# Optimization experiments

Measured on AMD Instinct MI355X. Metric: run time of the kernel, lower is better.

Reference implementation:

```python
import jax, jax.numpy as jnp
import numpy as np

KERNEL_SIZE = 7       # NMS max-pool window
H, W = 512, 1024      # dims
TOP_K = 200
CIRCLE_RADIUS = 5
NUM_CLASSES = 34      # things are labelIds 24..33


def _circle_constants(radius):
    k = 2 * radius + 1
    ii, jj = np.meshgrid(np.arange(k), np.arange(k), indexing='ij')
    ox = (jj - radius).astype(np.float32)  # x offset of neighbor
    oy = (ii - radius).astype(np.float32)  # y offset of neighbor
    cd = np.sqrt(ox ** 2 + oy ** 2)
    cmask = (cd <= radius).astype(np.float32)
    n_pix = float(cmask.sum())
    thr = float((cd * cmask).sum() / n_pix)  # center_threshold buffer
    return ox, oy, cmask, n_pix, thr


def _vote_map(center_regressions, radius):
    # For each pixel p, average over circle neighbors q = p + o of ||o - reg(q)||
    # (get_patches with zero padding), then vote = -avg - 1.
    ox, oy, cmask, n_pix, thr = _circle_constants(radius)
    B, _, h, w = center_regressions.shape
    reg_p = jnp.pad(center_regressions, ((0, 0), (0, 0), (radius, radius), (radius, radius)))
    acc = jnp.zeros((B, h, w), center_regressions.dtype)
    k = 2 * radius + 1
    for i in range(k):          # fixed 11x11 window, ~97 in-circle taps
        for j in range(k):
            if cmask[i, j] == 0.0:
                continue
            rx = reg_p[:, 0, i:i + h, j:j + w]
            ry = reg_p[:, 1, i:i + h, j:j + w]
            acc = acc + jnp.sqrt((ox[i, j] - rx) ** 2 + (oy[i, j] - ry) ** 2)
    vote = -(acc / n_pix) - 1.0  # [B,H,W], always <= -1
    return vote, thr


def _forward(segmentation_logits, center_regressions):
    B = segmentation_logits.shape[0]
    seg_probs = jax.nn.softmax(segmentation_logits, axis=1)                # [B,C,H,W]
    seg_map = jnp.argmax(segmentation_logits, axis=1).astype(jnp.float32)  # [B,H,W]
    # Threshold(23.99, 50) then <= 33  <=>  23.99 < class <= 33
    things = (seg_map > 23.99) & (seg_map <= 33.0)
    # predicted absolute center per pixel; xy_coords are 1-based
    xg = jnp.arange(1, W + 1, dtype=jnp.float32)[None, None, :]
    yg = jnp.arange(1, H + 1, dtype=jnp.float32)[None, :, None]
    px = xg - center_regressions[:, 0]                                     # [B,H,W]
    py = yg - center_regressions[:, 1]
    vote, thr = _vote_map(center_regressions, CIRCLE_RADIUS)
    pooled = jax.lax.reduce_window(vote, -jnp.inf, jax.lax.max,
                                   (1, KERNEL_SIZE, KERNEL_SIZE), (1, 1, 1), 'SAME')
    keep = (pooled == vote) & (vote > -thr - 1.0)
    center_map = jnp.where(keep, vote, 0.0)                                # nms-ed vote map
    # top-k centers: surviving NMS positions ranked by aggregate vote value
    scores = jnp.where(center_map != 0.0, vote, -jnp.inf).reshape(B, -1)
    top_vals, top_idx = jax.lax.top_k(scores, TOP_K)                       # [B,K]
    ys = top_idx // W
    xs = top_idx % W
    valid = jnp.isfinite(top_vals)
    BIG = 1e9
    cx = jnp.where(valid, xs.astype(jnp.float32), BIG)
    cy = jnp.where(valid, ys.astype(jnp.float32), BIG)
    # nearest-center assignment; squared distance (argmin invariant under sqrt)
    d2 = (px[..., None] - cx[:, None, None, :]) ** 2 + (py[..., None] - cy[:, None, None, :]) ** 2
    inst_map = (jnp.argmin(d2, axis=-1).astype(jnp.int32) + 1) * things.astype(jnp.int32)
    return seg_probs, seg_map, center_map, inst_map, ys, xs, top_vals


def _instance_stats(inst_map, seg_map, seg_probs):
    # separate_inst_maps: per instance -> majority seg class, mean prob of that
    # class over the instance mask, and pixel count (vectorized via segment_sum)
    B = inst_map.shape[0]
    seg_ids = seg_map.astype(jnp.int32).reshape(B, -1)                     # [B,HW]
    inst_flat = inst_map.reshape(B, -1)                                    # [B,HW], 0 = background
    onehot = jax.nn.one_hot(seg_ids, NUM_CLASSES, dtype=jnp.float32)       # [B,HW,C]
    probs = jnp.transpose(seg_probs, (0, 2, 3, 1)).reshape(B, -1, NUM_CLASSES)
    seg_counts = jax.vmap(lambda v, s: jax.ops.segment_sum(v, s, num_segments=TOP_K + 1))(onehot, inst_flat)
    prob_sums = jax.vmap(lambda v, s: jax.ops.segment_sum(v, s, num_segments=TOP_K + 1))(probs, inst_flat)
    seg_counts = seg_counts[:, 1:]                                         # drop background -> [B,K,C]
    prob_sums = prob_sums[:, 1:]
    inst_size = seg_counts.sum(-1)                                         # [B,K]
    inst_class = jnp.argmax(seg_counts, axis=-1).astype(jnp.int32)         # [B,K]
    sel = jnp.take_along_axis(prob_sums, inst_class[..., None], axis=-1)[..., 0]
    inst_seg_prob = sel / jnp.maximum(inst_size, 1.0)
    return inst_class, inst_seg_prob, inst_size.astype(jnp.int32)


def setup_inputs() -> dict:
    key = jax.random.key(0)
    k1, k2, k3 = jax.random.split(key, 3)
    return {
        'segmentation_logits': jax.random.normal(k1, (2, NUM_CLASSES, H, W), jnp.float32),
        'center_maps_placeholder': jax.random.normal(k2, (2, 1, H, W), jnp.float32),
        'center_regressions': jax.random.normal(k3, (2, 2, H, W), jnp.float32),
    }


def reference(segmentation_logits, center_maps_placeholder, center_regressions):
    seg_probs, seg_map, center_map, inst_map, ys, xs, top_vals = _forward(
        segmentation_logits, center_regressions)
    inst_class, inst_seg_prob, inst_size = _instance_stats(inst_map, seg_map, seg_probs)
    centers = jnp.stack([ys, xs], -1).astype(jnp.int32)  # (row, col) like torch.nonzero
    return (inst_map, seg_map, centers, top_vals, inst_class, inst_seg_prob, inst_size, center_map)
```

## Files before the change

### kernel.cpp

```cpp
#include <hip/hip_runtime.h>
#include <cfloat>
#include <cmath>

#define NB 2
#define NC 34
#define NH 512
#define NW 1024
#define HWSZ (NH*NW)
#define TK 200
#define CAPC 49152
#define ACH 1024
#define NTH 10
#define ZWORDS (8 + NB*TK*NTH)

#define PST 1040
#define RPROWS 522
#define RPLEFT 8
#define VPROWS 518
#define VPLEFT 4
#define RPSZ (RPROWS*PST)
#define VPSZ (VPROWS*PST)

typedef unsigned long long u64;

#define PREP_ROWB (NB*2*RPROWS)
#define PREP_VF4 ((NB*VPSZ)/4)
#define PREP_VB ((PREP_VF4 + 255)/256)
#define PREP_ZB ((ZWORDS + NB*TK + 255)/256 + 1)
__global__ __launch_bounds__(256) void k_prep(const float* __restrict__ reg,
                                              float* __restrict__ reg_pad,
                                              float* __restrict__ vote_pad,
                                              int* __restrict__ zreg,
                                              float* __restrict__ o_iprob) {
    int bid = blockIdx.x;
    int tid = threadIdx.x;
    if (bid < PREP_ROWB) {
        int bc = bid / RPROWS;
        int r = bid % RPROWS;
        float* dst = reg_pad + (size_t)bc * RPSZ + (size_t)r * PST;
        if (r >= 5 && r < 517) {
            const float* src = reg + (size_t)bc * HWSZ + (size_t)(r - 5) * NW;
            *(float4*)(dst + RPLEFT + 4 * tid) = *(const float4*)(src + 4 * tid);
            if (tid < 2) *(float4*)(dst + 4 * tid) = make_float4(0.f, 0.f, 0.f, 0.f);
            else if (tid < 4) *(float4*)(dst + 1032 + 4 * (tid - 2)) = make_float4(0.f, 0.f, 0.f, 0.f);
        } else {
            for (int i = tid; i < PST / 4; i += 256)
                *(float4*)(dst + 4 * i) = make_float4(0.f, 0.f, 0.f, 0.f);
        }
    } else if (bid < PREP_ROWB + PREP_VB) {
        int idx4 = (bid - PREP_ROWB) * 256 + tid;
        if (idx4 < PREP_VF4)
            *(float4*)(vote_pad + (size_t)idx4 * 4) = make_float4(-INFINITY, -INFINITY, -INFINITY, -INFINITY);
    } else {
        int z = (bid - (PREP_ROWB + PREP_VB)) * 256 + tid;
        if (z < ZWORDS) zreg[z] = 0;
        else if (z < ZWORDS + NB * TK) o_iprob[z - ZWORDS] = 0.f;
    }
}

#define GETC(f, idx) (((idx)&3)==0 ? f[(idx)>>2].x : ((idx)&3)==1 ? f[(idx)>>2].y : \
                      ((idx)&3)==2 ? f[(idx)>>2].z : f[(idx)>>2].w)

__global__ __launch_bounds__(256, 4) void k_vote_seg(const float* __restrict__ reg_pad,
                                                     float* __restrict__ vote_pad,
                                                     const float* __restrict__ logits,
                                                     float* __restrict__ segmap_out,
                                                     float* __restrict__ mArr,
                                                     float* __restrict__ dArr) {
    int tid = threadIdx.x;
    int blk = blockIdx.x;
    int b = blk >> 9;
    int q = blk & 511;
    int y = ((q & 7) << 6) | (q >> 3);
    int xb = tid << 2;
    const float* rp0 = reg_pad + (size_t)(b * 2 + 0) * RPSZ;
    const float* rp1 = reg_pad + (size_t)(b * 2 + 1) * RPSZ;
    float a0 = 0.f, a1 = 0.f, a2 = 0.f, a3 = 0.f;

    float4 fA0[5], fA1[5], fB0[5], fB1[5];

    auto loadwin = [&](int i, float4* f0, float4* f1) {
        const float* p0 = rp0 + (size_t)(y + i) * PST + xb;
        const float* p1 = rp1 + (size_t)(y + i) * PST + xb;
#pragma unroll
        for (int t = 0; t < 5; t++) f0[t] = *(const float4*)(p0 + 4 * t);
#pragma unroll
        for (int t = 0; t < 5; t++) f1[t] = *(const float4*)(p1 + 4 * t);
    };

    auto compute = [&](int i, const float4* f0, const float4* f1) {
        int d = i - 5;
        int ad = d < 0 ? -d : d;
        int w = (int)sqrtf((float)(25 - ad * ad));
        int lo = 5 - w, hi = 5 + w;
        float di = (float)d;
#pragma unroll
        for (int j = 0; j < 11; j++) {
            if (j < lo || j > hi) continue;
            float dj = (float)(j - 5);
            float dx, dy, ss;
            dx = __fsub_rn(dj, GETC(f0, j+3)); dy = __fsub_rn(di, GETC(f1, j+3));
            ss = __fadd_rn(__fmul_rn(dx,dx), __fmul_rn(dy,dy));
            a0 = __fadd_rn(a0, sqrtf(ss));
            dx = __fsub_rn(dj, GETC(f0, j+4)); dy = __fsub_rn(di, GETC(f1, j+4));
            ss = __fadd_rn(__fmul_rn(dx,dx), __fmul_rn(dy,dy));
            a1 = __fadd_rn(a1, sqrtf(ss));
            dx = __fsub_rn(dj, GETC(f0, j+5)); dy = __fsub_rn(di, GETC(f1, j+5));
            ss = __fadd_rn(__fmul_rn(dx,dx), __fmul_rn(dy,dy));
            a2 = __fadd_rn(a2, sqrtf(ss));
            dx = __fsub_rn(dj, GETC(f0, j+6)); dy = __fsub_rn(di, GETC(f1, j+6));
            ss = __fadd_rn(__fmul_rn(dx,dx), __fmul_rn(dy,dy));
            a3 = __fadd_rn(a3, sqrtf(ss));
        }
    };

    loadwin(0, fA0, fA1);
#pragma unroll 1
    for (int i = 0; i < 10; i += 2) {
        loadwin(i + 1, fB0, fB1);
        compute(i, fA0, fA1);
        loadwin(i + 2, fA0, fA1);
        compute(i + 1, fB0, fB1);
    }
    compute(10, fA0, fA1);

    float4 vv;
    vv.x = __fsub_rn(-__fdiv_rn(a0, 81.0f), 1.0f);
    vv.y = __fsub_rn(-__fdiv_rn(a1, 81.0f), 1.0f);
    vv.z = __fsub_rn(-__fdiv_rn(a2, 81.0f), 1.0f);
    vv.w = __fsub_rn(-__fdiv_rn(a3, 81.0f), 1.0f);
    *(float4*)(vote_pad + (size_t)b * VPSZ + (size_t)(y + 3) * PST + (xb + VPLEFT)) = vv;

    const float* lg = logits + (size_t)b * NC * HWSZ + (size_t)y * NW + xb;
    float4 m4 = make_float4(-FLT_MAX, -FLT_MAX, -FLT_MAX, -FLT_MAX);
    float4 bc4 = make_float4(0.f, 0.f, 0.f, 0.f);
#pragma unroll
    for (int c = 0; c < NC; c++) {
        float4 v = *(const float4*)(lg + (size_t)c * HWSZ);
        if (v.x > m4.x) { m4.x = v.x; bc4.x = (float)c; }
        if (v.y > m4.y) { m4.y = v.y; bc4.y = (float)c; }
        if (v.z > m4.z) { m4.z = v.z; bc4.z = (float)c; }
        if (v.w > m4.w) { m4.w = v.w; bc4.w = (float)c; }
    }
    float4 den = make_float4(0.f, 0.f, 0.f, 0.f);
#pragma unroll
    for (int c = 0; c < NC; c++) {
        float4 v = *(const float4*)(lg + (size_t)c * HWSZ);
        den.x += expf(v.x - m4.x);
        den.y += expf(v.y - m4.y);
        den.z += expf(v.z - m4.z);
        den.w += expf(v.w - m4.w);
    }
    size_t po = (size_t)b * HWSZ + (size_t)y * NW + xb;
    *(float4*)(segmap_out + po) = bc4;
    *(float4*)(mArr + po) = m4;
    *(float4*)(dArr + po) = den;
}

__global__ __launch_bounds__(256) void k_pool(const float* __restrict__ vote_pad,
                                              float* __restrict__ cmap_out,
                                              u64* __restrict__ keys,
                                              int* __restrict__ ccnt,
                                              float thr_keep) {
    int tid = threadIdx.x;
    int blk = blockIdx.x;
    int b = blk >> 9;
    int q = blk & 511;
    int y = ((q & 7) << 6) | (q >> 3);
    int xb = tid << 2;
    const float* vp = vote_pad + (size_t)b * VPSZ;
    float cm[10];
#pragma unroll
    for (int t = 0; t < 10; t++) cm[t] = -INFINITY;
    float vv[4];
#pragma unroll 1
    for (int dy = -3; dy <= 3; dy++) {
        const float* row = vp + (size_t)(y + dy + 3) * PST + xb;
        float4 A = *(const float4*)(row);
        float4 Bq = *(const float4*)(row + 4);
        float4 Cq = *(const float4*)(row + 8);
        float L[12] = {A.x,A.y,A.z,A.w, Bq.x,Bq.y,Bq.z,Bq.w, Cq.x,Cq.y,Cq.z,Cq.w};
#pragma unroll
        for (int t = 0; t < 10; t++) cm[t] = fmaxf(cm[t], L[t + 1]);
        if (dy == 0) { vv[0]=L[4]; vv[1]=L[5]; vv[2]=L[6]; vv[3]=L[7]; }
    }
    int pix = y * NW + xb;
    float cmap[4];
#pragma unroll
    for (int k = 0; k < 4; k++) {
        float mx = cm[k];
#pragma unroll
        for (int u = 1; u < 7; u++) mx = fmaxf(mx, cm[k+u]);
        bool keep = (mx == vv[k]) && (vv[k] > thr_keep);
        cmap[k] = keep ? vv[k] : 0.0f;
        if (keep) {
            int pos = atomicAdd(&ccnt[b], 1);
            if (pos < CAPC) {
                unsigned u = __float_as_uint(vv[k]);
                unsigned ou = ((int)u < 0) ? ~u : (u | 0x80000000u);
                keys[(size_t)b * CAPC + pos] = ((u64)ou << 19) | (u64)(HWSZ - 1 - (pix + k));
            }
        }
    }
    *(float4*)(cmap_out + b * HWSZ + pix) = make_float4(cmap[0],cmap[1],cmap[2],cmap[3]);
}

__device__ inline void bitonic_desc(u64* a, int np2, int tid, int T) {
    for (int k = 2; k <= np2; k <<= 1) {
        for (int j = k >> 1; j > 0; j >>= 1) {
            for (int i = tid; i < np2; i += T) {
                int ixj = i ^ j;
                if (ixj > i) {
                    u64 x = a[i], y = a[ixj];
                    bool up = ((i & k) == 0);
                    if (up ? (x < y) : (x > y)) { a[i] = y; a[ixj] = x; }
                }
            }
            __syncthreads();
        }
    }
}

__global__ __launch_bounds__(1024) void k_topk(const u64* __restrict__ keys_g,
                                               const int* __restrict__ ccnt,
                                               float* __restrict__ cxArr,
                                               float* __restrict__ cyArr,
                                               float* __restrict__ out_centers,
                                               float* __restrict__ out_topvals) {
    __shared__ int hist[2048];
    __shared__ int ssum[1024];
    __shared__ u64 sel[256];
    __shared__ int scnt;
    __shared__ int sB, sSab, scB;
    const int T = 1024;
    int b = blockIdx.x;
    int tid = threadIdx.x;
    int n = ccnt[b];
    if (n > CAPC) n = CAPC;
    const u64* Kg = keys_g + (size_t)b * CAPC;

    u64 thr;
    if (n <= TK) {
        thr = 1;
    } else {
        u64 prefixval = 0;
        int pbits = 0, need = TK;
        thr = 0;
        const int widths[5] = {11, 11, 11, 11, 7};
        bool done = false;
        for (int lvl = 0; lvl < 5 && !done; ++lvl) {
            int w = widths[lvl];
            int nb = 1 << w;
            int shift = 51 - pbits - w;
            for (int i = tid; i < nb; i += T) hist[i] = 0;
            __syncthreads();
            for (int i = tid; i < n; i += T) {
                u64 k = Kg[i];
                if ((k >> (51 - pbits)) == prefixval)
                    atomicAdd(&hist[(int)((k >> shift) & (u64)(nb - 1))], 1);
            }
            __syncthreads();
            int items = (nb + T - 1) / T;
            int sv = 0;
            for (int it = 0; it < items; ++it) {
                int j = tid * items + it;
                if (j < nb) sv += hist[j];
            }
            ssum[tid] = sv;
            __syncthreads();
            for (int off = 1; off < T; off <<= 1) {
                int v = (tid + off < T) ? ssum[tid + off] : 0;
                __syncthreads();
                ssum[tid] += v;
                __syncthreads();
            }
            int incl = ssum[tid];
            int excl = (tid + 1 < T) ? ssum[tid + 1] : 0;
            if (excl < need && need <= incl) {
                int acc = excl;
                int base2 = tid * items;
                for (int it = items - 1; it >= 0; --it) {
                    int j = base2 + it;
                    if (j >= nb) continue;
                    int h = hist[j];
                    if (acc + h >= need) { sB = j; sSab = acc; scB = h; break; }
                    acc += h;
                }
            }
            __syncthreads();
            int B = sB, Sab = sSab, cB = scB;
            int sel_total = (TK - need) + Sab;
            if (sel_total + cB <= 256) {
                thr = ((prefixval << w) | (u64)B) << shift;
                done = true;
            } else {
                prefixval = (prefixval << w) | (u64)B;
                pbits += w;
                need = need - Sab;
            }
            __syncthreads();
        }
    }

    if (tid == 0) scnt = 0;
    if (tid < 256) sel[tid] = 0;
    __syncthreads();
    for (int i = tid; i < n; i += T) {
        u64 k = Kg[i];
        if (k >= thr && k != 0ULL) {
            int p = atomicAdd(&scnt, 1);
            if (p < 256) sel[p] = k;
        }
    }
    __syncthreads();
    bitonic_desc(sel, 256, tid, T);
    if (tid < TK) {
        u64 w = sel[tid];
        bool valid = (w != 0ULL);
        unsigned ou = (unsigned)(w >> 19);
        unsigned ub = (ou & 0x80000000u) ? (ou & 0x7FFFFFFFu) : ~ou;
        float v = __uint_as_float(ub);
        int pix = valid ? (int)(HWSZ - 1 - (int)(w & 0x7FFFFULL)) : 0x7fffffff;
        int ys = pix >> 10;
        int xs = pix & (NW - 1);
        cxArr[b * TK + tid] = valid ? (float)xs : 1e9f;
        cyArr[b * TK + tid] = valid ? (float)ys : 1e9f;
        out_centers[(b * TK + tid) * 2 + 0] = (float)ys;
        out_centers[(b * TK + tid) * 2 + 1] = (float)xs;
        out_topvals[b * TK + tid] = valid ? v : -INFINITY;
    }
}

__global__ __launch_bounds__(256) void k_assign(const float* __restrict__ reg,
                                                const float* __restrict__ segmap,
                                                const float* __restrict__ cxArr,
                                                const float* __restrict__ cyArr,
                                                float* __restrict__ out_inst,
                                                int* __restrict__ segcnt) {
    __shared__ int lcnt[TK * NTH];
    __shared__ float swx[TK];
    __shared__ float swy[TK];
    __shared__ int swk[TK];
    __shared__ float sred[256];
    __shared__ int wcnt[4];
    __shared__ float sbox[4];

    int tid = threadIdx.x;
    int bid = blockIdx.x;
    int b = bid >> 9;
    int r = bid & 511;
    int ty = r >> 5, tx = r & 31;
    int y0 = ty << 5, x0 = tx << 5;
    int row = tid >> 3;
    int col = (tid & 7) << 2;
    int y = y0 + row;
    int x = x0 + col;
    int pix0 = (y << 10) + x;

    for (int t = tid; t < TK * NTH; t += 256) lcnt[t] = 0;

    const float* r0 = reg + (size_t)b * 2 * HWSZ;
    const float* r1 = r0 + HWSZ;
    float4 rx = *(const float4*)(r0 + pix0);
    float4 ry = *(const float4*)(r1 + pix0);
    float px[4], py[4];
    px[0] = __fsub_rn((float)(x + 1), rx.x); py[0] = __fsub_rn((float)(y + 1), ry.x);
    px[1] = __fsub_rn((float)(x + 2), rx.y); py[1] = __fsub_rn((float)(y + 1), ry.y);
    px[2] = __fsub_rn((float)(x + 3), rx.z); py[2] = __fsub_rn((float)(y + 1), ry.z);
    px[3] = __fsub_rn((float)(x + 4), rx.w); py[3] = __fsub_rn((float)(y + 1), ry.w);

    float pxlo = fminf(fminf(px[0], px[1]), fminf(px[2], px[3]));
    float pxhi = fmaxf(fmaxf(px[0], px[1]), fmaxf(px[2], px[3]));
    float pylo = fminf(fminf(py[0], py[1]), fminf(py[2], py[3]));
    float pyhi = fmaxf(fmaxf(py[0], py[1]), fmaxf(py[2], py[3]));
#pragma unroll
    for (int off = 32; off >= 1; off >>= 1) {
        pxlo = fminf(pxlo, __shfl_xor(pxlo, off));
        pxhi = fmaxf(pxhi, __shfl_xor(pxhi, off));
        pylo = fminf(pylo, __shfl_xor(pylo, off));
        pyhi = fmaxf(pyhi, __shfl_xor(pyhi, off));
    }
    int wid = tid >> 6;
    int lane = tid & 63;
    if (lane == 0) {
        sred[wid * 4 + 0] = pxlo; sred[wid * 4 + 1] = pxhi;
        sred[wid * 4 + 2] = pylo; sred[wid * 4 + 3] = pyhi;
    }
    __syncthreads();
    if (tid == 0) {
        float a = sred[0], bq = sred[1], c = sred[2], d = sred[3];
        for (int w = 1; w < 4; w++) {
            a  = fminf(a,  sred[w * 4 + 0]);
            bq = fmaxf(bq, sred[w * 4 + 1]);
            c  = fminf(c,  sred[w * 4 + 2]);
            d  = fmaxf(d,  sred[w * 4 + 3]);
        }
        sbox[0] = a; sbox[1] = bq; sbox[2] = c; sbox[3] = d;
    }
    __syncthreads();
    float bxlo = sbox[0], bxhi = sbox[1], bylo = sbox[2], byhi = sbox[3];

    float Lk = 0.f, Uk = INFINITY, cxv = 0.f, cyv = 0.f;
    if (tid < TK) {
        cxv = cxArr[b * TK + tid];
        cyv = cyArr[b * TK + tid];
        float dl = fmaxf(fmaxf(__fsub_rn(bxlo, cxv), __fsub_rn(cxv, bxhi)), 0.f);
        float el = fmaxf(fmaxf(__fsub_rn(bylo, cyv), __fsub_rn(cyv, byhi)), 0.f);
        float du = fmaxf(__fsub_rn(cxv, bxlo), __fsub_rn(bxhi, cxv));
        float eu = fmaxf(__fsub_rn(cyv, bylo), __fsub_rn(byhi, cyv));
        Lk = __fadd_rn(__fmul_rn(dl, dl), __fmul_rn(el, el));
        Uk = __fadd_rn(__fmul_rn(du, du), __fmul_rn(eu, eu));
    }
    sred[tid] = Uk;
    __syncthreads();
#pragma unroll
    for (int s = 128; s > 0; s >>= 1) {
        if (tid < s) sred[tid] = fminf(sred[tid], sred[tid + s]);
        __syncthreads();
    }
    float Umin = sred[0];

    bool flag = (tid < TK) && (Lk <= Umin);
    u64 mask = __ballot(flag);
    int wpre = __popcll(mask & ((1ULL << lane) - 1ULL));
    if (lane == 0) wcnt[wid] = (int)__popcll(mask);
    __syncthreads();
    int base_off = 0;
#pragma unroll
    for (int w = 0; w < 4; w++) if (w < wid) base_off += wcnt[w];
    int m = wcnt[0] + wcnt[1] + wcnt[2] + wcnt[3];
    if (flag) {
        int p = base_off + wpre;
        swx[p] = cxv; swy[p] = cyv; swk[p] = tid;
    }
    __syncthreads();

    float bd[4]; int bk[4];
#pragma unroll
    for (int it = 0; it < 4; it++) { bd[it] = INFINITY; bk[it] = 0; }
    for (int k2 = 0; k2 < m; k2++) {
        float cx = swx[k2];
        float cy = swy[k2];
        int kk = swk[k2];
#pragma unroll
        for (int it = 0; it < 4; it++) {
            float dx = __fsub_rn(px[it], cx);
            float dy = __fsub_rn(py[it], cy);
            float d2 = __fadd_rn(__fmul_rn(dx, dx), __fmul_rn(dy, dy));
            if (d2 < bd[it]) { bd[it] = d2; bk[it] = kk; }
        }
    }

    float4 sm = *(const float4*)(segmap + (size_t)b * HWSZ + pix0);
    float scls[4] = {sm.x, sm.y, sm.z, sm.w};
    float oi[4];
#pragma unroll
    for (int it = 0; it < 4; it++) {
        int cls = (int)scls[it];
        int thing = (cls >= 24) ? 1 : 0;
        int inst = (bk[it] + 1) * thing;
        oi[it] = (float)inst;
        if (inst) atomicAdd(&lcnt[bk[it] * NTH + (cls - 24)], 1);
    }
    *(float4*)(out_inst + (size_t)b * HWSZ + pix0) = make_float4(oi[0], oi[1], oi[2], oi[3]);
    __syncthreads();
    for (int t = tid; t < TK * NTH; t += 256) {
        int v = lcnt[t];
        if (v) atomicAdd(&segcnt[b * TK * NTH + t], v);
    }
}

__global__ __launch_bounds__(256) void k_statsprob(const float* __restrict__ logits,
                                                   const float* __restrict__ inst_f,
                                                   const float* __restrict__ mArr,
                                                   const float* __restrict__ dArr,
                                                   const int* __restrict__ segcnt,
                                                   float* __restrict__ out_icls,
                                                   float* __restrict__ out_isize,
                                                   float* __restrict__ out_iprob) {
    __shared__ float lps[TK];
    __shared__ int sicls[TK];
    __shared__ float ssz[TK];
    int tid = threadIdx.x;
    int base = blockIdx.x * ACH;
    int b = base >> 19;
    if (tid < TK) {
        const int* rowp = segcnt + (size_t)(b * TK + tid) * NTH;
        int total = 0, bc = 0, bv = -1;
#pragma unroll
        for (int c = 0; c < NTH; c++) {
            int v = rowp[c];
            total += v;
            if (v > bv) { bv = v; bc = c; }
        }
        int cls = (total == 0) ? 0 : (24 + bc);
        sicls[tid] = cls;
        ssz[tid] = fmaxf((float)total, 1.0f);
        if ((blockIdx.x & 511) == 0) {
            out_icls[b * TK + tid] = (float)cls;
            out_isize[b * TK + tid] = (float)total;
        }
    }
    for (int t = tid; t < TK; t += 256) lps[t] = 0.f;
    __syncthreads();
    int p0 = base + tid * 4;
    float4 fi = *(const float4*)(inst_f + p0);
    float4 fm = *(const float4*)(mArr + p0);
    float4 fd = *(const float4*)(dArr + p0);
    float insts[4] = {fi.x, fi.y, fi.z, fi.w};
    float ms[4] = {fm.x, fm.y, fm.z, fm.w};
    float ds[4] = {fd.x, fd.y, fd.z, fd.w};
#pragma unroll
    for (int it = 0; it < 4; it++) {
        int inst = (int)insts[it];
        if (inst) {
            int p = p0 + it;
            int pix = p & (HWSZ - 1);
            int c = sicls[inst - 1];
            float xv = logits[(size_t)(b * NC + c) * HWSZ + pix];
            float pr = __fdiv_rn(expf(__fsub_rn(xv, ms[it])), ds[it]);
            atomicAdd(&lps[inst - 1], pr);
        }
    }
    __syncthreads();
    for (int t = tid; t < TK; t += 256) {
        float s = lps[t];
        if (s != 0.f) {
            float sz = ssz[t];
            atomicAdd(&out_iprob[b * TK + t], s / sz);
        }
    }
}

static float compute_thr_keep() {
    float cdm[121];
    int t = 0;
    for (int i = 0; i < 11; i++) {
        for (int j = 0; j < 11; j++) {
            float ox = (float)(j - 5), oy = (float)(i - 5);
            float cd = sqrtf(ox * ox + oy * oy);
            float cm = (cd <= 5.0f) ? 1.0f : 0.0f;
            cdm[t++] = cd * cm;
        }
    }
    float r[8];
    for (int k = 0; k < 8; k++) r[k] = cdm[k];
    int i = 8;
    for (; i < 121 - (121 % 8); i += 8)
        for (int k = 0; k < 8; k++) r[k] += cdm[i + k];
    float res = ((r[0] + r[1]) + (r[2] + r[3])) + ((r[4] + r[5]) + (r[6] + r[7]));
    for (; i < 121; i++) res += cdm[i];
    float thr = res / 81.0f;
    double kt = -(double)thr - 1.0;
    return (float)kt;
}

extern "C" void kernel_launch(void* const* d_in, const int* in_sizes, int n_in,
                              void* d_out, int out_size, void* d_ws, size_t ws_size,
                              hipStream_t stream) {
    const float* logits = (const float*)d_in[0];
    const float* reg    = (const float*)d_in[2];
    float* out = (float*)d_out;

    float* o_inst    = out;
    float* o_seg     = out + 1048576;
    float* o_centers = out + 2097152;
    float* o_topvals = out + 2097952;
    float* o_icls    = out + 2098352;
    float* o_iprob   = out + 2098752;
    float* o_isize   = out + 2099152;
    float* o_cmap    = out + 2099552;

    u64* keys = (u64*)d_ws;
    float* wsf = (float*)(keys + (size_t)NB * CAPC);
    size_t o = 0;
    int*   zreg    = (int*)(wsf + o); o += ZWORDS;
    int*   ccnt    = zreg;
    int*   segcnt  = zreg + 8;
    float* reg_pad = wsf + o; o += (size_t)NB * 2 * RPSZ;
    float* vote_pad= wsf + o; o += (size_t)NB * VPSZ;
    float* mArr    = wsf + o; o += (size_t)NB * HWSZ;
    float* dArr    = wsf + o; o += (size_t)NB * HWSZ;
    float* cxArr   = wsf + o; o += NB * TK;
    float* cyArr   = wsf + o; o += NB * TK;

    float thr_keep = compute_thr_keep();

    int gridPrep = PREP_ROWB + PREP_VB + PREP_ZB;
    int gridRow = NB * NH;
    int gridAgg = (NB * HWSZ) / ACH;

    k_prep<<<gridPrep, 256, 0, stream>>>(reg, reg_pad, vote_pad, zreg, o_iprob);
    k_vote_seg<<<gridRow, 256, 0, stream>>>(reg_pad, vote_pad, logits, o_seg, mArr, dArr);
    k_pool<<<gridRow, 256, 0, stream>>>(vote_pad, o_cmap, keys, ccnt, thr_keep);
    k_topk<<<NB, 1024, 0, stream>>>(keys, ccnt, cxArr, cyArr, o_centers, o_topvals);
    k_assign<<<gridAgg, 256, 0, stream>>>(reg, o_seg, cxArr, cyArr, o_inst, segcnt);
    k_statsprob<<<gridAgg, 256, 0, stream>>>(logits, o_inst, mArr, dArr, segcnt, o_icls, o_isize, o_iprob);
}
```

Measured before the change: 379.7 us.

## Split softmax stats into separate blocks and fill only vote_pad borders

```diff
diff --git a/kernel.cpp b/kernel.cpp
--- a/kernel.cpp
+++ b/kernel.cpp
@@ -24,8 +24,8 @@
 typedef unsigned long long u64;
 
 #define PREP_ROWB (NB*2*RPROWS)
-#define PREP_VF4 ((NB*VPSZ)/4)
-#define PREP_VB ((PREP_VF4 + 255)/256)
+#define PREP_BR (NB*6)
+#define PREP_ST 16
 #define PREP_ZB ((ZWORDS + NB*TK + 255)/256 + 1)
 __global__ __launch_bounds__(256) void k_prep(const float* __restrict__ reg,
                                               float* __restrict__ reg_pad,
@@ -34,6 +34,7 @@
                                               float* __restrict__ o_iprob) {
     int bid = blockIdx.x;
     int tid = threadIdx.x;
+    const float4 NEG4 = make_float4(-INFINITY, -INFINITY, -INFINITY, -INFINITY);
     if (bid < PREP_ROWB) {
         int bc = bid / RPROWS;
         int r = bid % RPROWS;
@@ -47,12 +48,24 @@
             for (int i = tid; i < PST / 4; i += 256)
                 *(float4*)(dst + 4 * i) = make_float4(0.f, 0.f, 0.f, 0.f);
         }
-    } else if (bid < PREP_ROWB + PREP_VB) {
-        int idx4 = (bid - PREP_ROWB) * 256 + tid;
-        if (idx4 < PREP_VF4)
-            *(float4*)(vote_pad + (size_t)idx4 * 4) = make_float4(-INFINITY, -INFINITY, -INFINITY, -INFINITY);
+    } else if (bid < PREP_ROWB + PREP_BR) {
+        int bid2 = bid - PREP_ROWB;
+        int bb = bid2 / 6;
+        int rsel = bid2 % 6;
+        int r = (rsel < 3) ? rsel : (512 + rsel);
+        float* dst = vote_pad + (size_t)bb * VPSZ + (size_t)r * PST;
+        for (int i = tid; i < PST / 4; i += 256)
+            *(float4*)(dst + 4 * i) = NEG4;
+    } else if (bid < PREP_ROWB + PREP_BR + PREP_ST) {
+        int idx = (bid - PREP_ROWB - PREP_BR) * 256 + tid;
+        int bb = idx >> 11;
+        int rem = idx & 2047;
+        int r = 3 + (rem >> 2);
+        int s = rem & 3;
+        int f4 = (s == 0) ? 0 : (256 + s);
+        *(float4*)(vote_pad + (size_t)bb * VPSZ + (size_t)r * PST + 4 * f4) = NEG4;
     } else {
-        int z = (bid - (PREP_ROWB + PREP_VB)) * 256 + tid;
+        int z = (bid - (PREP_ROWB + PREP_BR + PREP_ST)) * 256 + tid;
         if (z < ZWORDS) zreg[z] = 0;
         else if (z < ZWORDS + NB * TK) o_iprob[z - ZWORDS] = 0.f;
     }
@@ -61,6 +74,8 @@
 #define GETC(f, idx) (((idx)&3)==0 ? f[(idx)>>2].x : ((idx)&3)==1 ? f[(idx)>>2].y : \
                       ((idx)&3)==2 ? f[(idx)>>2].z : f[(idx)>>2].w)
 
+#define VOTEB (NB*NH)
+#define SEGB  ((NB*HWSZ)/256)
 __global__ __launch_bounds__(256, 4) void k_vote_seg(const float* __restrict__ reg_pad,
                                                      float* __restrict__ vote_pad,
                                                      const float* __restrict__ logits,
@@ -68,7 +83,27 @@
                                                      float* __restrict__ mArr,
                                                      float* __restrict__ dArr) {
     int tid = threadIdx.x;
-    int blk = blockIdx.x;
+    int bid = blockIdx.x;
+    if (bid >= VOTEB) {
+        int p = (bid - VOTEB) * 256 + tid;
+        int b = p >> 19;
+        int pix = p & (HWSZ - 1);
+        const float* basep = logits + (size_t)b * NC * HWSZ + pix;
+        float v[NC];
+#pragma unroll
+        for (int c = 0; c < NC; c++) v[c] = basep[(size_t)c * HWSZ];
+        float m = -FLT_MAX; int bc = 0;
+#pragma unroll
+        for (int c = 0; c < NC; c++) { if (v[c] > m) { m = v[c]; bc = c; } }
+        float den = 0.f;
+#pragma unroll
+        for (int c = 0; c < NC; c++) den += expf(v[c] - m);
+        segmap_out[p] = (float)bc;
+        mArr[p] = m;
+        dArr[p] = den;
+        return;
+    }
+    int blk = bid;
     int b = blk >> 9;
     int q = blk & 511;
     int y = ((q & 7) << 6) | (q >> 3);
@@ -130,31 +165,6 @@
     vv.z = __fsub_rn(-__fdiv_rn(a2, 81.0f), 1.0f);
     vv.w = __fsub_rn(-__fdiv_rn(a3, 81.0f), 1.0f);
     *(float4*)(vote_pad + (size_t)b * VPSZ + (size_t)(y + 3) * PST + (xb + VPLEFT)) = vv;
-
-    const float* lg = logits + (size_t)b * NC * HWSZ + (size_t)y * NW + xb;
-    float4 m4 = make_float4(-FLT_MAX, -FLT_MAX, -FLT_MAX, -FLT_MAX);
-    float4 bc4 = make_float4(0.f, 0.f, 0.f, 0.f);
-#pragma unroll
-    for (int c = 0; c < NC; c++) {
-        float4 v = *(const float4*)(lg + (size_t)c * HWSZ);
-        if (v.x > m4.x) { m4.x = v.x; bc4.x = (float)c; }
-        if (v.y > m4.y) { m4.y = v.y; bc4.y = (float)c; }
-        if (v.z > m4.z) { m4.z = v.z; bc4.z = (float)c; }
-        if (v.w > m4.w) { m4.w = v.w; bc4.w = (float)c; }
-    }
-    float4 den = make_float4(0.f, 0.f, 0.f, 0.f);
-#pragma unroll
-    for (int c = 0; c < NC; c++) {
-        float4 v = *(const float4*)(lg + (size_t)c * HWSZ);
-        den.x += expf(v.x - m4.x);
-        den.y += expf(v.y - m4.y);
-        den.z += expf(v.z - m4.z);
-        den.w += expf(v.w - m4.w);
-    }
-    size_t po = (size_t)b * HWSZ + (size_t)y * NW + xb;
-    *(float4*)(segmap_out + po) = bc4;
-    *(float4*)(mArr + po) = m4;
-    *(float4*)(dArr + po) = den;
 }
 
 __global__ __launch_bounds__(256) void k_pool(const float* __restrict__ vote_pad,
@@ -586,12 +596,13 @@
 
     float thr_keep = compute_thr_keep();
 
-    int gridPrep = PREP_ROWB + PREP_VB + PREP_ZB;
+    int gridPrep = PREP_ROWB + PREP_BR + PREP_ST + PREP_ZB;
+    int gridVS = VOTEB + SEGB;
     int gridRow = NB * NH;
     int gridAgg = (NB * HWSZ) / ACH;
 
     k_prep<<<gridPrep, 256, 0, stream>>>(reg, reg_pad, vote_pad, zreg, o_iprob);
-    k_vote_seg<<<gridRow, 256, 0, stream>>>(reg_pad, vote_pad, logits, o_seg, mArr, dArr);
+    k_vote_seg<<<gridVS, 256, 0, stream>>>(reg_pad, vote_pad, logits, o_seg, mArr, dArr);
     k_pool<<<gridRow, 256, 0, stream>>>(vote_pad, o_cmap, keys, ccnt, thr_keep);
     k_topk<<<NB, 1024, 0, stream>>>(keys, ccnt, cxArr, cyArr, o_centers, o_topvals);
     k_assign<<<gridAgg, 256, 0, stream>>>(reg, o_seg, cxArr, cyArr, o_inst, segcnt);
```

Result: faster. 346.8 us (-8.7%).
